# Performance work log

Hardware: AMD Instinct MI355X
Metric: run time of the kernel (lower is better)

The kernel has to match this reference:

```python
import jax, jax.numpy as jnp
import numpy as np
from jax import lax

DT = 0.001
DX = 0.02
H = 2048
P = 256


def _lap(u):
    # 5-point Laplacian numerator on interior: u[2:,1:-1]-4u[1:-1,1:-1]+u[:-2,1:-1]+u[1:-1,2:]+u[1:-1,:-2]
    return (u[:, :, 2:, 1:-1] - 4.0 * u[:, :, 1:-1, 1:-1] + u[:, :, :-2, 1:-1]
            + u[:, :, 1:-1, 2:] + u[:, :, 1:-1, :-2])


def setup_inputs() -> dict:
    key = jax.random.key(0)
    ks = jax.random.split(key, 8)
    inp = {
        "ref_speed": jax.random.uniform(ks[0], (1, 1, H, H), jnp.float32, 0.1, 1.0),
        "batch": jax.random.normal(ks[1], (12, 1, H, H), jnp.float32),
        "x_tt": jax.random.normal(ks[2], (1, 1, H, H), jnp.float32),
        "x_t": jax.random.normal(ks[3], (1, 1, H, H), jnp.float32),
        "ref_sol": jax.random.normal(ks[4], (16, 1, H, H), jnp.float32),
        "conv_v": jax.random.normal(ks[5], (1, 3, 3, 3), jnp.float32) * np.sqrt(1.0 / (3 * 3 * 320)),
        "conv_g": jax.random.uniform(ks[6], (1,), jnp.float32, 0.5, 1.5),
        "conv_b": jax.random.normal(ks[7], (1,), jnp.float32) * 0.01,
        "loc_x": jax.random.randint(jax.random.fold_in(key, 10), (P,), 0, H),
        "loc_y": jax.random.randint(jax.random.fold_in(key, 11), (P,), 0, H),
        "bsize": 10,
        "id": 1,
        "flag": 1,
        "flag_num": 1,
    }
    return inp


def reference(ref_speed, batch, x_tt, x_t, ref_sol, conv_v, conv_g, conv_b,
              loc_x, loc_y, bsize, id, flag, flag_num):
    sg = lax.stop_gradient
    ntb = flag - 1
    step = flag_num - 1

    xtt = sg(batch[ntb * bsize + step: ntb * bsize + step + 1])   # [1,1,H,W]
    xt = sg(batch[ntb * bsize + step + 1: ntb * bsize + step + 2])

    coef = sg(ref_speed[:, :, 1:-1, 1:-1]) ** 2 * (DT ** 2) / (DX ** 2)

    # explicit FD step (outputs3)
    x_t4 = jnp.zeros_like(xt)
    x_t4 = x_t4.at[:, :, 1:-1, 1:-1].set(
        2.0 * xt[:, :, 1:-1, 1:-1] - xtt[:, :, 1:-1, 1:-1] + _lap(xt) * coef)

    # weight-normed 3x3 conv (3->1 channels, padding=1)
    vnorm = jnp.sqrt(jnp.sum(conv_v ** 2, axis=(1, 2, 3), keepdims=True))
    W = conv_g.reshape(-1, 1, 1, 1) * conv_v / vnorm
    x_t1 = jnp.concatenate([xtt, xt, ref_speed], axis=1)  # [1,3,H,W]
    y = lax.conv_general_dilated(x_t1, W, (1, 1), ((1, 1), (1, 1)),
                                 dimension_numbers=("NCHW", "OIHW", "NCHW"))
    y = y + conv_b.reshape(1, -1, 1, 1)

    # stencil update on conv output interior (RHS evaluated from pre-assignment y)
    x7 = y.at[:, :, 1:-1, 1:-1].set(
        2.0 * xt[:, :, 1:-1, 1:-1] - xtt[:, :, 1:-1, 1:-1] + _lap(y) * coef)
    x7_pre = x7  # clone captured into outputs2 before boundary edits

    # boundaries, in original order
    x7 = x7.at[:, :, 0, :].set(0.0)
    left = xt[:, :, :, 0:1] - DT * sg(ref_speed[:, :, :, 0:1]) * (xt[:, :, :, 0:1] - xt[:, :, :, 1:2]) / DX
    x7 = x7.at[:, :, :, 0:1].set(left)
    rows = jnp.arange(1, H - 1)
    cols = H - rows
    x7 = x7.at[:, :, rows, cols].set(xt[:, :, rows - 1, cols - 1])
    right = xt[:, :, :, -1:] - DT * sg(ref_speed[:, :, :, -1:]) * (xt[:, :, :, -1:] - xt[:, :, :, -2:-1]) / DX
    x7 = x7.at[:, :, :, -1:].set(right)
    x7 = x7.at[:, :, -1, :].set(0.0)

    # per-point observation scatter from ref_sol (-1 entries skipped)
    obs = ref_sol[id * bsize + step + 2: id * bsize + step + 3]  # [1,1,H,W]
    valid = loc_x != -1
    lx = jnp.where(valid, loc_x, 0)
    ly = jnp.where(valid, loc_y, 0)
    vals = obs[:, :, lx, ly]          # [1,1,P]
    cur = x7[:, :, lx, ly]
    x7 = x7.at[:, :, lx, ly].set(jnp.where(valid[None, None, :], vals, cur))

    outputs1 = jnp.concatenate([x_tt, x_t, x7], axis=0)       # [3,1,H,W]
    outputs2 = jnp.concatenate([x_tt, x_t, x7_pre], axis=0)   # [3,1,H,W]
    return jnp.concatenate([outputs1, outputs2, x_t4], axis=0)  # [7,1,H,W]
```

## Files before the change

### kernel.cpp

```cpp
#include <hip/hip_runtime.h>

#define HD 2048
#define HH (HD*HD)

__device__ __forceinline__ float coef_of(float rs) { return rs * rs * 0.0025f; }

__global__ __launch_bounds__(256) void conv_y_kernel(
    const float* __restrict__ batch,
    const float* __restrict__ rs,
    const float* __restrict__ conv_v,
    const float* __restrict__ conv_g,
    const float* __restrict__ conv_b,
    const int* __restrict__ p_bsize,
    const int* __restrict__ p_flag,
    const int* __restrict__ p_flagnum,
    float* __restrict__ y)
{
    int idx = blockIdx.x * blockDim.x + threadIdx.x;
    if (idx >= HH) return;
    int i = idx >> 11;
    int j = idx & (HD - 1);

    int base = ((p_flag[0] - 1) * p_bsize[0] + (p_flagnum[0] - 1)) * HH;
    const float* __restrict__ xtt = batch + base;
    const float* __restrict__ xt  = batch + base + HH;

    float ss = 0.f;
    float w[27];
    #pragma unroll
    for (int k = 0; k < 27; ++k) { w[k] = conv_v[k]; ss += w[k] * w[k]; }
    float scale = conv_g[0] / sqrtf(ss);

    float acc = conv_b[0];
    #pragma unroll
    for (int kh = 0; kh < 3; ++kh) {
        int ii = i + kh - 1;
        if (ii < 0 || ii >= HD) continue;
        #pragma unroll
        for (int kw = 0; kw < 3; ++kw) {
            int jj = j + kw - 1;
            if (jj < 0 || jj >= HD) continue;
            int o = ii * HD + jj;
            acc += scale * (w[kh * 3 + kw]      * xtt[o]
                          + w[9 + kh * 3 + kw]  * xt[o]
                          + w[18 + kh * 3 + kw] * rs[o]);
        }
    }
    y[idx] = acc;
}

__global__ __launch_bounds__(256) void main_kernel(
    const float* __restrict__ batch,
    const float* __restrict__ rs,
    const float* __restrict__ x_tt_in,
    const float* __restrict__ x_t_in,
    const float* __restrict__ y,
    const int* __restrict__ p_bsize,
    const int* __restrict__ p_flag,
    const int* __restrict__ p_flagnum,
    float* __restrict__ out)
{
    int idx = blockIdx.x * blockDim.x + threadIdx.x;
    if (idx >= HH) return;
    int i = idx >> 11;
    int j = idx & (HD - 1);

    int base = ((p_flag[0] - 1) * p_bsize[0] + (p_flagnum[0] - 1)) * HH;
    const float* __restrict__ xtt = batch + base;
    const float* __restrict__ xt  = batch + base + HH;

    float a_tt = x_tt_in[idx];
    float a_t  = x_t_in[idx];
    out[idx]            = a_tt;
    out[HH + idx]       = a_t;
    out[3 * HH + idx]   = a_tt;
    out[4 * HH + idx]   = a_t;

    float xc = xt[idx];
    float xo = xtt[idx];
    float rc = rs[idx];
    float yc = y[idx];

    bool interior = (i > 0) & (i < HD - 1) & (j > 0) & (j < HD - 1);

    float xt4 = 0.f;
    float ypre;
    if (interior) {
        float coef = coef_of(rc);
        float lapx = xt[idx - HD] + xt[idx + HD] + xt[idx - 1] + xt[idx + 1] - 4.f * xc;
        xt4 = 2.f * xc - xo + lapx * coef;
        float lapy = y[idx - HD] + y[idx + HD] + y[idx - 1] + y[idx + 1] - 4.f * yc;
        ypre = 2.f * xc - xo + lapy * coef;
    } else {
        ypre = yc;
    }
    out[6 * HH + idx] = xt4;
    out[5 * HH + idx] = ypre;

    float v = ypre;
    if (i == 0) v = 0.f;
    if (j == 0) {
        float x1 = xt[i * HD + 1];
        v = xc - 0.05f * rc * (xc - x1);
    }
    if (i >= 1 && i <= HD - 2 && j == HD - i) {
        v = xt[(i - 1) * HD + (j - 1)];
    }
    if (j == HD - 1) {
        float x1 = xt[i * HD + HD - 2];
        v = xc - 0.05f * rc * (xc - x1);
    }
    if (i == HD - 1) v = 0.f;
    out[2 * HH + idx] = v;
}

__global__ __launch_bounds__(256) void scatter_kernel(
    const float* __restrict__ ref_sol,
    const int* __restrict__ loc_x,
    const int* __restrict__ loc_y,
    const int* __restrict__ p_bsize,
    const int* __restrict__ p_id,
    const int* __restrict__ p_flagnum,
    float* __restrict__ out)
{
    int k = blockIdx.x * blockDim.x + threadIdx.x;
    if (k >= 256) return;
    int lx = loc_x[k];
    if (lx == -1) return;
    int ly = loc_y[k];
    int off = (p_id[0] * p_bsize[0] + (p_flagnum[0] - 1) + 2) * HH;
    out[2 * HH + lx * HD + ly] = ref_sol[off + lx * HD + ly];
}

extern "C" void kernel_launch(void* const* d_in, const int* in_sizes, int n_in,
                              void* d_out, int out_size, void* d_ws, size_t ws_size,
                              hipStream_t stream) {
    const float* ref_speed = (const float*)d_in[0];
    const float* batch     = (const float*)d_in[1];
    const float* x_tt      = (const float*)d_in[2];
    const float* x_t       = (const float*)d_in[3];
    const float* ref_sol   = (const float*)d_in[4];
    const float* conv_v    = (const float*)d_in[5];
    const float* conv_g    = (const float*)d_in[6];
    const float* conv_b    = (const float*)d_in[7];
    const int*   loc_x     = (const int*)d_in[8];
    const int*   loc_y     = (const int*)d_in[9];
    const int*   bsize     = (const int*)d_in[10];
    const int*   id        = (const int*)d_in[11];
    const int*   flag      = (const int*)d_in[12];
    const int*   flag_num  = (const int*)d_in[13];

    float* out = (float*)d_out;
    float* y   = (float*)d_ws;

    dim3 block(256);
    dim3 grid((HH + 255) / 256);

    conv_y_kernel<<<grid, block, 0, stream>>>(batch, ref_speed, conv_v, conv_g, conv_b,
                                              bsize, flag, flag_num, y);
    main_kernel<<<grid, block, 0, stream>>>(batch, ref_speed, x_tt, x_t, y,
                                            bsize, flag, flag_num, out);
    scatter_kernel<<<1, 256, 0, stream>>>(ref_sol, loc_x, loc_y, bsize, id, flag_num, out);
}
```

Before: 499.5 us.

## Fuse conv and stencil kernels with shared-memory tiles and halos

Merges the weight-normed conv kernel and the stencil/boundary kernel into one tiled kernel. Each block stages xt with a 2-pixel halo in LDS, computes the conv output y for the tile plus a 1-pixel halo into LDS, then evaluates the Laplacians and boundaries from LDS. This removes the global y round trip and an extra launch, at the cost of recomputing the conv on halos and adding LDS traffic and syncs.

```diff
diff --git a/kernel.cpp b/kernel.cpp
--- a/kernel.cpp
+++ b/kernel.cpp
@@ -1,117 +1,131 @@
 #include <hip/hip_runtime.h>
 
-#define HD 2048
-#define HH (HD*HD)
+#define HD   2048
+#define HHW  (HD*HD)
+#define TX   64
+#define TY   32
+#define XSTR 68
+#define XROWS 36
+#define YROWS 34
+#define YCOLS 66
 
-__device__ __forceinline__ float coef_of(float rs) { return rs * rs * 0.0025f; }
 
-__global__ __launch_bounds__(256) void conv_y_kernel(
+__global__ __launch_bounds__(256) void fused_kernel(
     const float* __restrict__ batch,
     const float* __restrict__ rs,
+    const float* __restrict__ x_tt_in,
+    const float* __restrict__ x_t_in,
     const float* __restrict__ conv_v,
     const float* __restrict__ conv_g,
     const float* __restrict__ conv_b,
     const int* __restrict__ p_bsize,
     const int* __restrict__ p_flag,
     const int* __restrict__ p_flagnum,
-    float* __restrict__ y)
+    float* __restrict__ out)
 {
-    int idx = blockIdx.x * blockDim.x + threadIdx.x;
-    if (idx >= HH) return;
-    int i = idx >> 11;
-    int j = idx & (HD - 1);
+    __shared__ float xts[XROWS * XSTR];
+    __shared__ float ys [YROWS * XSTR];
 
-    int base = ((p_flag[0] - 1) * p_bsize[0] + (p_flagnum[0] - 1)) * HH;
+    const int tid = threadIdx.x;
+    const int gi0 = blockIdx.y * TY;
+    const int gj0 = blockIdx.x * TX;
+
+    const int base = ((p_flag[0] - 1) * p_bsize[0] + (p_flagnum[0] - 1)) * HHW;
     const float* __restrict__ xtt = batch + base;
-    const float* __restrict__ xt  = batch + base + HH;
+    const float* __restrict__ xt  = batch + base + HHW;
 
+    float w[27];
     float ss = 0.f;
-    float w[27];
     #pragma unroll
     for (int k = 0; k < 27; ++k) { w[k] = conv_v[k]; ss += w[k] * w[k]; }
-    float scale = conv_g[0] / sqrtf(ss);
+    const float scale = conv_g[0] / sqrtf(ss);
+    const float bias  = conv_b[0];
 
-    float acc = conv_b[0];
-    #pragma unroll
-    for (int kh = 0; kh < 3; ++kh) {
-        int ii = i + kh - 1;
-        if (ii < 0 || ii >= HD) continue;
+    for (int p = tid; p < XROWS * XSTR; p += 256) {
+        int li = p / XSTR;
+        int lj = p - li * XSTR;
+        int gi = gi0 - 2 + li;
+        int gj = gj0 - 2 + lj;
+        float v = 0.f;
+        if ((unsigned)gi < HD && (unsigned)gj < HD) v = xt[gi * HD + gj];
+        xts[p] = v;
+    }
+    __syncthreads();
+
+    for (int p = tid; p < YROWS * YCOLS; p += 256) {
+        int li = p / YCOLS;
+        int lj = p - li * YCOLS;
+        int gi = gi0 - 1 + li;
+        int gj = gj0 - 1 + lj;
+        if ((unsigned)gi >= HD || (unsigned)gj >= HD) continue;
+        float acc = 0.f;
         #pragma unroll
-        for (int kw = 0; kw < 3; ++kw) {
-            int jj = j + kw - 1;
-            if (jj < 0 || jj >= HD) continue;
-            int o = ii * HD + jj;
-            acc += scale * (w[kh * 3 + kw]      * xtt[o]
-                          + w[9 + kh * 3 + kw]  * xt[o]
-                          + w[18 + kh * 3 + kw] * rs[o]);
+        for (int kh = 0; kh < 3; ++kh) {
+            int ii = gi + kh - 1;
+            bool rok = (unsigned)ii < HD;
+            const float* rowt = xtt + ii * HD;
+            const float* rowr = rs  + ii * HD;
+            #pragma unroll
+            for (int kw = 0; kw < 3; ++kw) {
+                int jj = gj + kw - 1;
+                bool ok = rok && ((unsigned)jj < HD);
+                float t0 = ok ? rowt[jj] : 0.f;
+                float t1 = xts[(li + kh) * XSTR + lj + kw];
+                float t2 = ok ? rowr[jj] : 0.f;
+                acc += w[kh * 3 + kw]      * t0
+                     + w[9 + kh * 3 + kw]  * t1
+                     + w[18 + kh * 3 + kw] * t2;
+            }
         }
+        ys[li * XSTR + lj] = bias + scale * acc;
     }
-    y[idx] = acc;
-}
+    __syncthreads();
 
-__global__ __launch_bounds__(256) void main_kernel(
-    const float* __restrict__ batch,
-    const float* __restrict__ rs,
-    const float* __restrict__ x_tt_in,
-    const float* __restrict__ x_t_in,
-    const float* __restrict__ y,
-    const int* __restrict__ p_bsize,
-    const int* __restrict__ p_flag,
-    const int* __restrict__ p_flagnum,
-    float* __restrict__ out)
-{
-    int idx = blockIdx.x * blockDim.x + threadIdx.x;
-    if (idx >= HH) return;
-    int i = idx >> 11;
-    int j = idx & (HD - 1);
+    const int c  = tid & 63;
+    const int rg = tid >> 6;
+    for (int k = 0; k < 8; ++k) {
+        int row = rg * 8 + k;
+        int gi  = gi0 + row;
+        int gj  = gj0 + c;
+        int idx = gi * HD + gj;
 
-    int base = ((p_flag[0] - 1) * p_bsize[0] + (p_flagnum[0] - 1)) * HH;
-    const float* __restrict__ xtt = batch + base;
-    const float* __restrict__ xt  = batch + base + HH;
+        float a_tt = x_tt_in[idx];
+        float a_t  = x_t_in[idx];
+        float xc = xts[(row + 2) * XSTR + c + 2];
+        float xo = xtt[idx];
+        float rc = rs[idx];
+        float yc = ys[(row + 1) * XSTR + c + 1];
 
-    float a_tt = x_tt_in[idx];
-    float a_t  = x_t_in[idx];
-    out[idx]            = a_tt;
-    out[HH + idx]       = a_t;
-    out[3 * HH + idx]   = a_tt;
-    out[4 * HH + idx]   = a_t;
+        bool interior = (gi > 0) & (gi < HD - 1) & (gj > 0) & (gj < HD - 1);
+        float xt4 = 0.f, ypre;
+        if (interior) {
+            float coef = rc * rc * 0.0025f;
+            float lapx = xts[(row + 1) * XSTR + c + 2] + xts[(row + 3) * XSTR + c + 2]
+                       + xts[(row + 2) * XSTR + c + 1] + xts[(row + 2) * XSTR + c + 3] - 4.f * xc;
+            xt4 = 2.f * xc - xo + lapx * coef;
+            float lapy = ys[row * XSTR + c + 1] + ys[(row + 2) * XSTR + c + 1]
+                       + ys[(row + 1) * XSTR + c] + ys[(row + 1) * XSTR + c + 2] - 4.f * yc;
+            ypre = 2.f * xc - xo + lapy * coef;
+        } else {
+            ypre = yc;
+        }
 
-    float xc = xt[idx];
-    float xo = xtt[idx];
-    float rc = rs[idx];
-    float yc = y[idx];
+        float v = ypre;
+        if (gi == 0) v = 0.f;
+        if (gj == 0)      v = xc - 0.05f * rc * (xc - xts[(row + 2) * XSTR + 3]);
+        if (gi >= 1 && gi <= HD - 2 && gj == HD - gi)
+                          v = xts[(row + 1) * XSTR + c + 1];
+        if (gj == HD - 1) v = xc - 0.05f * rc * (xc - xts[(row + 2) * XSTR + c + 1]);
+        if (gi == HD - 1) v = 0.f;
 
-    bool interior = (i > 0) & (i < HD - 1) & (j > 0) & (j < HD - 1);
-
-    float xt4 = 0.f;
-    float ypre;
-    if (interior) {
-        float coef = coef_of(rc);
-        float lapx = xt[idx - HD] + xt[idx + HD] + xt[idx - 1] + xt[idx + 1] - 4.f * xc;
-        xt4 = 2.f * xc - xo + lapx * coef;
-        float lapy = y[idx - HD] + y[idx + HD] + y[idx - 1] + y[idx + 1] - 4.f * yc;
-        ypre = 2.f * xc - xo + lapy * coef;
-    } else {
-        ypre = yc;
+        out[idx]            = a_tt;
+        out[HHW + idx]      = a_t;
+        out[2 * HHW + idx]  = v;
+        out[3 * HHW + idx]  = a_tt;
+        out[4 * HHW + idx]  = a_t;
+        out[5 * HHW + idx]  = ypre;
+        out[6 * HHW + idx]  = xt4;
     }
-    out[6 * HH + idx] = xt4;
-    out[5 * HH + idx] = ypre;
-
-    float v = ypre;
-    if (i == 0) v = 0.f;
-    if (j == 0) {
-        float x1 = xt[i * HD + 1];
-        v = xc - 0.05f * rc * (xc - x1);
-    }
-    if (i >= 1 && i <= HD - 2 && j == HD - i) {
-        v = xt[(i - 1) * HD + (j - 1)];
-    }
-    if (j == HD - 1) {
-        float x1 = xt[i * HD + HD - 2];
-        v = xc - 0.05f * rc * (xc - x1);
-    }
-    if (i == HD - 1) v = 0.f;
-    out[2 * HH + idx] = v;
 }
 
 __global__ __launch_bounds__(256) void scatter_kernel(
@@ -128,8 +142,8 @@
     int lx = loc_x[k];
     if (lx == -1) return;
     int ly = loc_y[k];
-    int off = (p_id[0] * p_bsize[0] + (p_flagnum[0] - 1) + 2) * HH;
-    out[2 * HH + lx * HD + ly] = ref_sol[off + lx * HD + ly];
+    int off = (p_id[0] * p_bsize[0] + (p_flagnum[0] - 1) + 2) * HHW;
+    out[2 * HHW + lx * HD + ly] = ref_sol[off + lx * HD + ly];
 }
 
 extern "C" void kernel_launch(void* const* d_in, const int* in_sizes, int n_in,
@@ -151,14 +165,12 @@
     const int*   flag_num  = (const int*)d_in[13];
 
     float* out = (float*)d_out;
-    float* y   = (float*)d_ws;
 
     dim3 block(256);
-    dim3 grid((HH + 255) / 256);
+    dim3 grid(HD / TX, HD / TY);
 
-    conv_y_kernel<<<grid, block, 0, stream>>>(batch, ref_speed, conv_v, conv_g, conv_b,
-                                              bsize, flag, flag_num, y);
-    main_kernel<<<grid, block, 0, stream>>>(batch, ref_speed, x_tt, x_t, y,
-                                            bsize, flag, flag_num, out);
+    fused_kernel<<<grid, block, 0, stream>>>(batch, ref_speed, x_tt, x_t,
+                                             conv_v, conv_g, conv_b,
+                                             bsize, flag, flag_num, out);
     scatter_kernel<<<1, 256, 0, stream>>>(ref_sol, loc_x, loc_y, bsize, id, flag_num, out);
 }
```

Measured after the change: 492.5 us. Within noise of the previous version (-1.4%).
